# Performance work log

Measured on AMD Instinct MI355X. Metric: run time of the kernel, lower is better.

Reference implementation:

```python
import jax, jax.numpy as jnp
import numpy as np

N_T = 200
THR = 0.6
ALPHA = 0.8   # hard-coded in __init__
KAPPA = 0.8   # hard-coded in __init__
RHO = 0.97
BETA = 0.07
SCALE = 50.0  # get_pos scale
# norse defaults used by ConstantCurrentLIFEncoder / LILinearCell
DT = 1e-3
TAU_MEM_INV = 100.0
TAU_SYN_INV = 200.0
V_TH = 1.0


def encode_constant_current(I):
    """norse ConstantCurrentLIFEncoder: LIF driven by constant current I [n_b, f] -> spikes [n_t, n_b, f]."""
    def step(v, _):
        v = v + DT * TAU_MEM_INV * (I - v)          # dv = dt*tau_mem_inv*((v_leak - v) + I), v_leak=0
        z = (v > V_TH).astype(I.dtype)
        v = v * (1.0 - z)                            # reset to v_reset=0 on spike
        return v, z
    _, zs = jax.lax.scan(step, jnp.zeros_like(I), None, length=N_T)
    return zs


def setup_inputs() -> dict:
    key = jax.random.key(0)
    ks = jax.random.split(key, 5)
    n_b, n_feat = 128, 512
    n_in, n_rec, n_out = 2 * n_feat, 2048, 32
    x = jax.random.normal(ks[0], (n_b, n_feat), jnp.float32)
    # kaiming_normal_ std = sqrt(2/fan_in), then scaled by w_init_gain
    w_in = jax.random.normal(ks[1], (n_rec, n_in), jnp.float32) * (0.5 * np.sqrt(2.0 / n_in))
    w_rec = jax.random.normal(ks[2], (n_rec, n_rec), jnp.float32) * (0.1 * np.sqrt(2.0 / n_rec))
    w_out = jax.random.normal(ks[3], (n_out, n_rec), jnp.float32) * (0.5 * np.sqrt(2.0 / n_rec))
    w_li = jax.random.normal(ks[4], (1, n_rec), jnp.float32) * np.sqrt(2.0 / n_rec)
    return {"x": x, "w_in": w_in, "w_rec": w_rec, "w_out": w_out, "w_li": w_li}


def reference(x, w_in, w_rec, w_out, w_li):
    n_rec = w_rec.shape[0]
    n_out = w_out.shape[0]
    n_b = x.shape[0]
    # get_pos: pos/neg rectified constant-current LIF encoding, cat on feature dim -> [n_t, n_b, n_in]
    xs = jnp.concatenate([
        encode_constant_current(jax.nn.relu(SCALE * x)),
        encode_constant_current(jax.nn.relu(-SCALE * x)),
    ], axis=2)
    # zero self-recurrence: w_rec *= (1 - I)
    w_rec = w_rec * (1.0 - jnp.eye(n_rec, dtype=w_rec.dtype))

    def step(carry, x_t):
        v, a, z, vo, li_v, li_i = carry
        # ALIF membrane update + adaptive threshold spike
        v = ALPHA * v + z @ w_rec.T + x_t @ w_in.T - z * THR
        a = RHO * a + z
        z = (v > THR + BETA * a).astype(v.dtype)
        # (dropout p=0.5 treated as identity / eval mode)
        vo = KAPPA * vo + z @ w_out.T
        # norse LILinearCell critic readout (li_step)
        i_jump = li_i + z @ w_li.T
        li_v = li_v + DT * TAU_MEM_INV * (i_jump - li_v)
        li_i = i_jump - DT * TAU_SYN_INV * i_jump
        return (v, a, z, vo, li_v, li_i), (vo, li_v)

    zeros = lambda d: jnp.zeros((n_b, d), x.dtype)
    carry0 = (zeros(n_rec), zeros(n_rec), zeros(n_rec), zeros(n_out), zeros(1), zeros(1))
    _, (vo_seq, vc_seq) = jax.lax.scan(step, carry0, xs[: N_T - 1])  # loop runs n_t-1 steps
    # torch.max over time includes the all-zero t=0 row -> clamp max with 0
    m = jnp.maximum(jnp.max(vo_seq, axis=0), 0.0)          # [n_b, n_out]
    yo = jax.nn.softmax(m, axis=1)
    critic_value = jnp.maximum(jnp.max(vc_seq, axis=0), 0.0)  # [n_b, 1]
    return yo, critic_value
```

## Files before the change

kernel.cpp:

```cpp
#include <hip/hip_runtime.h>
#include <cstdint>
#include <cstddef>

typedef __attribute__((ext_vector_type(8))) short short8;
typedef __attribute__((ext_vector_type(4))) float f32x4;
typedef __attribute__((ext_vector_type(4))) unsigned int u32x4;

union U4S8 { u32x4 u; short8 s; unsigned w[4]; };

#define TSTEPS 199

#define WF_PLANE 786432u
#define WR_BASE  1572864u
#define WR_PLANE 12288u

#define WS_BAR  0u
#define WS_ZB   4096u
#define WS_FIN  135168u
#define WS_XSB  151552u
#define WS_WF   3411968u
#define WS_NEED 28971008u

#define AT_RLX __ATOMIC_RELAXED
#define SC_AGT __HIP_MEMORY_SCOPE_AGENT

extern "C" __global__ __launch_bounds__(1024) void k_encode(
    const float* __restrict__ x, unsigned char* __restrict__ xsb)
{
  const int b = blockIdx.x;
  const int tid = threadIdx.x;
  const float xv = (tid < 512) ? x[b * 512 + tid] : x[b * 512 + tid - 512];
  const float I = (tid < 512) ? fmaxf(__fmul_rn(50.0f, xv), 0.0f)
                              : fmaxf(__fmul_rn(-50.0f, xv), 0.0f);
  float v = 0.0f;
  unsigned long long* dst =
      (unsigned long long*)(xsb + (size_t)b * 128u + (size_t)(tid >> 6) * 8u);
  for (int t = 0; t < TSTEPS; ++t) {
    v = __fadd_rn(v, __fmul_rn(0.1f, __fsub_rn(I, v)));
    const bool z = v > 1.0f;
    if (z) v = 0.0f;
    const unsigned long long m = __ballot(z ? 1 : 0);
    if ((tid & 63) == 0) dst[(size_t)t * 2048u] = m;
  }
}

__device__ __forceinline__ unsigned bf16rne(float f) {
  const unsigned u = __float_as_uint(f);
  return ((u + 0x7FFFu + ((u >> 16) & 1u)) >> 16) & 0xFFFFu;
}

extern "C" __global__ __launch_bounds__(256) void k_prep(
    const float* __restrict__ w_rec, const float* __restrict__ w_in,
    const float* __restrict__ w_out, const float* __restrict__ w_li,
    u32x4* __restrict__ wf)
{
  const unsigned idx  = blockIdx.x * 256u + threadIdx.x;
  const unsigned lane = idx & 63u;
  if (idx < 786432u) {
    const unsigned kt = (idx >> 6) % 96u;
    const unsigned ns = idx / 6144u;
    const unsigned j  = ns * 16u + (lane & 15u);
    const unsigned k0 = kt * 32u + (lane >> 4) * 8u;
    unsigned hi[4], lo[4];
#pragma unroll
    for (int u2 = 0; u2 < 4; ++u2) {
      unsigned hb[2], lb[2];
#pragma unroll
      for (int c = 0; c < 2; ++c) {
        const unsigned k = k0 + 2u * (unsigned)u2 + (unsigned)c;
        float w;
        if (k < 2048u) w = (k == j) ? 0.0f : w_rec[(size_t)j * 2048u + k];
        else           w = w_in[(size_t)j * 1024u + (k - 2048u)];
        const unsigned h = bf16rne(w);
        const float hvf = __uint_as_float(h << 16);
        const unsigned l = bf16rne(__fsub_rn(w, hvf));
        hb[c] = h; lb[c] = l;
      }
      hi[u2] = hb[0] | (hb[1] << 16);
      lo[u2] = lb[0] | (lb[1] << 16);
    }
    u32x4 vh, vl;
    vh[0]=hi[0]; vh[1]=hi[1]; vh[2]=hi[2]; vh[3]=hi[3];
    vl[0]=lo[0]; vl[1]=lo[1]; vl[2]=lo[2]; vl[3]=lo[3];
    wf[idx] = vh;
    wf[idx + WF_PLANE] = vl;
  } else if (idx < 786432u + 12288u) {
    const unsigned r   = idx - 786432u;
    const unsigned kt  = (r >> 6) & 63u;
    const unsigned nsr = r >> 12;
    const unsigned o   = nsr * 16u + (lane & 15u);
    const unsigned k0  = kt * 32u + (lane >> 4) * 8u;
    unsigned hi[4], lo[4];
#pragma unroll
    for (int u2 = 0; u2 < 4; ++u2) {
      unsigned hb[2], lb[2];
#pragma unroll
      for (int c = 0; c < 2; ++c) {
        const unsigned k = k0 + 2u * (unsigned)u2 + (unsigned)c;
        float w = 0.0f;
        if (o < 32u)       w = w_out[(size_t)o * 2048u + k];
        else if (o == 32u) w = w_li[k];
        const unsigned h = bf16rne(w);
        const float hvf = __uint_as_float(h << 16);
        hb[c] = h;
        lb[c] = bf16rne(__fsub_rn(w, hvf));
      }
      hi[u2] = hb[0] | (hb[1] << 16);
      lo[u2] = lb[0] | (lb[1] << 16);
    }
    u32x4 vh, vl;
    vh[0]=hi[0]; vh[1]=hi[1]; vh[2]=hi[2]; vh[3]=hi[3];
    vl[0]=lo[0]; vl[1]=lo[1]; vl[2]=lo[2]; vl[3]=lo[3];
    wf[WR_BASE + r] = vh;
    wf[WR_BASE + WR_PLANE + r] = vl;
  }
}

__device__ __forceinline__ void bar_arrive(unsigned* dbar, unsigned ns)
{
  __syncthreads();
  if (threadIdx.x == 0) {
    const unsigned prev = __hip_atomic_fetch_add(dbar + (ns >> 4) * 16u, 1u, AT_RLX, SC_AGT);
    if ((prev & 15u) == 15u) {
      const unsigned p2 = __hip_atomic_fetch_add(dbar + 128u, 1u, AT_RLX, SC_AGT);
      if ((p2 & 7u) == 7u)
        __hip_atomic_store(dbar + 144u, (p2 >> 3) + 1u, AT_RLX, SC_AGT);
    }
  }
}

__device__ __forceinline__ void bar_wait(unsigned* dbar, unsigned tgt)
{
  if (threadIdx.x == 0) {
    while (__hip_atomic_load(dbar + 144u, AT_RLX, SC_AGT) < tgt) {
      __builtin_amdgcn_s_sleep(1);
    }
    asm volatile("" ::: "memory");
  }
  __syncthreads();
}

extern "C" __global__ __launch_bounds__(512) void k_main(
    const u32x4* __restrict__ wf,
    const unsigned char* __restrict__ xsb,
    unsigned* __restrict__ zb,
    unsigned* __restrict__ bar,
    unsigned* __restrict__ fin,
    float* __restrict__ out)
{
  __shared__ unsigned abytes[64][100];
  __shared__ float red[8][64][17];
  __shared__ unsigned char zn[64][4];
  __shared__ float pad_lds[6000];

  const unsigned tid  = threadIdx.x;
  const unsigned wg   = blockIdx.x;
  const unsigned mh   = wg >> 7;
  const unsigned ns   = wg & 127u;
  const unsigned wv   = tid >> 6;
  const unsigned lane = tid & 63u;
  const unsigned ln15 = lane & 15u;
  const unsigned g4   = lane >> 4;
  const unsigned selr = g4 * 0x01010101u;
  const unsigned blq  = tid & 63u;
  const unsigned q    = tid >> 6;
  const bool     upd  = tid < 256u;
  const bool     dual = ns < 3u;

  if (tid == 0) ((volatile float*)pad_lds)[0] = 0.f;

  unsigned* dbar = bar + mh * 256u;

  const u32x4* WH = wf + (size_t)ns * 6144u;
  const u32x4* WL = wf + WF_PLANE + (size_t)ns * 6144u;
  const u32x4* RH = wf + WR_BASE + (size_t)ns * 4096u;
  const u32x4* RL = wf + WR_BASE + WR_PLANE + (size_t)ns * 4096u;

  float v[4]  = {0,0,0,0}, a[4] = {0,0,0,0}, zf[4] = {0,0,0,0};
  float vo[4] = {0,0,0,0}, voMax[4] = {0,0,0,0};
  float liv = 0.f, lii = 0.f, liMax = 0.f;

  f32x4 accX0 = {0,0,0,0}, accX1 = {0,0,0,0}, accX2 = {0,0,0,0}, accX3 = {0,0,0,0};
  U4S8 bhZ[8], blZ[8];
  const int zk = (int)wv * 8;
  const int xk = 64 + (int)wv * 4;

  auto stage_z = [&](unsigned buf) {
    const unsigned base = (buf * 2u + mh) * 64u * 128u;
    for (unsigned i = tid; i < 4096u; i += 512u) {
      const unsigned row = i >> 6, np = i & 63u;
      const unsigned long long vz = __hip_atomic_load(
          (const unsigned long long*)(zb + base + row * 128u + np * 2u),
          AT_RLX, SC_AGT);
      abytes[row][np] = (unsigned)(vz & 0xFFFFu) | (unsigned)(((vz >> 32) & 0xFFFFu) << 16);
    }
  };

  auto stage_xs = [&](int t) {
    const unsigned char* xr = xsb + ((size_t)t * 128u + mh * 64u) * 128u;
    for (unsigned i = tid; i < 2048u; i += 512u) {
      const unsigned row = i >> 5, c = i & 31u;
      abytes[row][64u + c] = *(const unsigned*)(xr + (size_t)row * 128u + c * 4u);
    }
  };

  auto mk = [&](unsigned dw, U4S8& af) {
    const unsigned sp = __builtin_amdgcn_perm(dw, dw, selr);
    const unsigned W  = ((sp >> 1) & 0xFFFF0000u) | (sp & 0x0000FFFFu);
    af.w[0] = __umul24(W & 0x00010001u, 0x3F80u);
    af.w[1] = __umul24(W & 0x00040004u, 0x0FE0u);
    af.w[2] = __umul24(W & 0x00100010u, 0x03F8u);
    af.w[3] = __umul24(W & 0x00400040u, 0x00FEu);
  };

  auto dosub2 = [&](unsigned dw, const short8& bhj, const short8& blj, f32x4& ACC) {
    U4S8 af; mk(dw, af);
    ACC = __builtin_amdgcn_mfma_f32_16x16x32_bf16(af.s, bhj, ACC, 0, 0, 0);
    ACC = __builtin_amdgcn_mfma_f32_16x16x32_bf16(af.s, blj, ACC, 0, 0, 0);
  };

  auto ldw = [&](const u32x4* H, const u32x4* L, int kb, U4S8* bh, U4S8* bl) {
#pragma unroll
    for (int j = 0; j < 4; ++j) {
      bh[j].u = H[(size_t)(kb + j) * 64u + lane];
      bl[j].u = L[(size_t)(kb + j) * 64u + lane];
    }
  };

  auto grp4 = [&](int kb, const U4S8* bh, const U4S8* bl) {
    U4S8 a0, a1, a2, a3;
    a0.u = *(const u32x4*)&abytes[ 0 + ln15][kb];
    a1.u = *(const u32x4*)&abytes[16 + ln15][kb];
    a2.u = *(const u32x4*)&abytes[32 + ln15][kb];
    a3.u = *(const u32x4*)&abytes[48 + ln15][kb];
#pragma unroll
    for (int j = 0; j < 4; ++j) {
      dosub2(a0.w[j], bh[j].s, bl[j].s, accX0);
      dosub2(a1.w[j], bh[j].s, bl[j].s, accX1);
      dosub2(a2.w[j], bh[j].s, bl[j].s, accX2);
      dosub2(a3.w[j], bh[j].s, bl[j].s, accX3);
    }
  };

  auto compute_accX = [&]() {
    U4S8 bh2[4], bl2[4];
    accX0 = {0,0,0,0}; accX1 = {0,0,0,0}; accX2 = {0,0,0,0}; accX3 = {0,0,0,0};
    ldw(WH, WL, xk, bh2, bl2);
    grp4(xk, bh2, bl2);
  };

  auto prefetchZ = [&]() {
#pragma unroll
    for (int j = 0; j < 8; ++j) {
      bhZ[j].u = WH[(size_t)(zk + j) * 64u + lane];
      blZ[j].u = WL[(size_t)(zk + j) * 64u + lane];
    }
  };

  auto zpart = [&]() {
    grp4(zk,     &bhZ[0], &blZ[0]);
    grp4(zk + 4, &bhZ[4], &blZ[4]);
  };

  auto redstore = [&]() {
#pragma unroll
    for (int r = 0; r < 4; ++r) {
      red[wv][ 0 + g4 * 4 + r][ln15] = accX0[r];
      red[wv][16 + g4 * 4 + r][ln15] = accX1[r];
      red[wv][32 + g4 * 4 + r][ln15] = accX2[r];
      red[wv][48 + g4 * 4 + r][ln15] = accX3[r];
    }
  };

  auto readout_pass = [&]() {
    f32x4 r0 = {0,0,0,0}, r1 = {0,0,0,0}, r2 = {0,0,0,0}, r3 = {0,0,0,0};
    const int kb = (int)wv * 8;
#pragma unroll
    for (int kc = 0; kc < 8; kc += 4) {
      U4S8 ar0, ar1, ar2, ar3;
      ar0.u = *(const u32x4*)&abytes[ 0 + ln15][kb + kc];
      ar1.u = *(const u32x4*)&abytes[16 + ln15][kb + kc];
      ar2.u = *(const u32x4*)&abytes[32 + ln15][kb + kc];
      ar3.u = *(const u32x4*)&abytes[48 + ln15][kb + kc];
      U4S8 bh[4], bl[4];
#pragma unroll
      for (int j = 0; j < 4; ++j) {
        bh[j].u = RH[(size_t)(kb + kc + j) * 64u + lane];
        bl[j].u = RL[(size_t)(kb + kc + j) * 64u + lane];
      }
#pragma unroll
      for (int j = 0; j < 4; ++j) {
        dosub2(ar0.w[j], bh[j].s, bl[j].s, r0);
        dosub2(ar1.w[j], bh[j].s, bl[j].s, r1);
        dosub2(ar2.w[j], bh[j].s, bl[j].s, r2);
        dosub2(ar3.w[j], bh[j].s, bl[j].s, r3);
      }
    }
#pragma unroll
    for (int r = 0; r < 4; ++r) {
      red[wv][ 0 + g4 * 4 + r][ln15] = r0[r];
      red[wv][16 + g4 * 4 + r][ln15] = r1[r];
      red[wv][32 + g4 * 4 + r][ln15] = r2[r];
      red[wv][48 + g4 * 4 + r][ln15] = r3[r];
    }
    __syncthreads();
    if (upd) {
      if (ns < 2u) {
#pragma unroll
        for (int jj = 0; jj < 4; ++jj) {
          const unsigned n = q * 4u + (unsigned)jj;
          float s = ((red[0][blq][n] + red[1][blq][n]) + (red[2][blq][n] + red[3][blq][n]))
                  + ((red[4][blq][n] + red[5][blq][n]) + (red[6][blq][n] + red[7][blq][n]));
          vo[jj] = __fadd_rn(__fmul_rn(0.8f, vo[jj]), s);
          voMax[jj] = fmaxf(voMax[jj], vo[jj]);
        }
      } else if (q == 0u) {
        float s = ((red[0][blq][0] + red[1][blq][0]) + (red[2][blq][0] + red[3][blq][0]))
                + ((red[4][blq][0] + red[5][blq][0]) + (red[6][blq][0] + red[7][blq][0]));
        const float ij = __fadd_rn(lii, s);
        liv = __fadd_rn(liv, __fmul_rn(0.1f, __fsub_rn(ij, liv)));
        lii = __fsub_rn(ij, __fmul_rn(0.2f, ij));
        liMax = fmaxf(liMax, liv);
      }
    }
    __syncthreads();
  };

  stage_xs(0);
  __syncthreads();
  compute_accX();
  prefetchZ();

  for (int t = 0; t < TSTEPS; ++t) {
    if (t > 0) bar_wait(dbar, (unsigned)t);
    stage_z((unsigned)t & 1u);
    __syncthreads();

    zpart();
    redstore();
    __syncthreads();

    if (upd) {
      unsigned nib = 0u;
#pragma unroll
      for (int jj = 0; jj < 4; ++jj) {
        const unsigned n = q * 4u + (unsigned)jj;
        const float dv = ((red[0][blq][n] + red[1][blq][n]) + (red[2][blq][n] + red[3][blq][n]))
                       + ((red[4][blq][n] + red[5][blq][n]) + (red[6][blq][n] + red[7][blq][n]));
        const float vv = __fsub_rn(__fadd_rn(__fmul_rn(0.8f, v[jj]), dv),
                                   __fmul_rn(zf[jj], 0.6f));
        a[jj] = __fadd_rn(__fmul_rn(0.97f, a[jj]), zf[jj]);
        const float th = __fadd_rn(0.6f, __fmul_rn(0.07f, a[jj]));
        const bool znew = vv > th;
        zf[jj] = znew ? 1.0f : 0.0f;
        v[jj] = vv;
        nib |= (znew ? 1u : 0u) << jj;
      }
      zn[blq][q] = (unsigned char)nib;
    }
    __syncthreads();

    if (tid < 64u) {
      const unsigned m16 = (unsigned)zn[tid][0] | ((unsigned)zn[tid][1] << 4) |
                           ((unsigned)zn[tid][2] << 8) | ((unsigned)zn[tid][3] << 12);
      const unsigned nb = ((unsigned)t & 1u) ^ 1u;
      __hip_atomic_store(zb + ((nb * 2u + mh) * 64u + tid) * 128u + ns, m16,
                         AT_RLX, SC_AGT);
    }
    bar_arrive(dbar, ns);

    if (t < TSTEPS - 1) stage_xs(t + 1);
    if (dual && t > 0) readout_pass();
    __syncthreads();
    if (t < TSTEPS - 1) {
      compute_accX();
      prefetchZ();
    }
  }

  bar_wait(dbar, (unsigned)TSTEPS);
  if (dual) {
    stage_z((unsigned)TSTEPS & 1u);
    __syncthreads();
    readout_pass();
    if (ns < 2u && upd) {
#pragma unroll
      for (int jj = 0; jj < 4; ++jj) {
        __hip_atomic_store(fin + ((size_t)mh * 64u + blq) * 32u + ns * 16u + q * 4u + (unsigned)jj,
                           __float_as_uint(voMax[jj]), AT_RLX, SC_AGT);
      }
    }
    if (ns == 2u && tid < 64u) {
      out[4096u + mh * 64u + tid] = liMax;
    }
  }
  bar_arrive(dbar, ns);

  if (ns == 0u) {
    bar_wait(dbar, (unsigned)TSTEPS + 1u);
    if (tid < 64u) {
      const unsigned grow = mh * 64u + tid;
      float vals[32];
#pragma unroll
      for (int o = 0; o < 32; ++o)
        vals[o] = __uint_as_float(__hip_atomic_load(fin + (size_t)grow * 32u + o,
                                                    AT_RLX, SC_AGT));
      float mx = vals[0];
#pragma unroll
      for (int o = 1; o < 32; ++o) mx = fmaxf(mx, vals[o]);
      float ssum = 0.f;
#pragma unroll
      for (int o = 0; o < 32; ++o) ssum += expf(vals[o] - mx);
      const float inv = 1.0f / ssum;
#pragma unroll
      for (int o = 0; o < 32; ++o) out[(size_t)grow * 32u + o] = expf(vals[o] - mx) * inv;
    }
  }
}

extern "C" void kernel_launch(void* const* d_in, const int* in_sizes, int n_in,
                              void* d_out, int out_size, void* d_ws, size_t ws_size,
                              hipStream_t stream)
{
  (void)in_sizes; (void)n_in; (void)out_size;
  if (ws_size < (size_t)WS_NEED) return;

  const float* x     = (const float*)d_in[0];
  const float* w_in  = (const float*)d_in[1];
  const float* w_rec = (const float*)d_in[2];
  const float* w_out = (const float*)d_in[3];
  const float* w_li  = (const float*)d_in[4];
  unsigned char* ws  = (unsigned char*)d_ws;

  unsigned*      bar  = (unsigned*)(ws + WS_BAR);
  unsigned*      zb   = (unsigned*)(ws + WS_ZB);
  unsigned*      fin  = (unsigned*)(ws + WS_FIN);
  unsigned char* xsb  = ws + WS_XSB;
  u32x4*         wf   = (u32x4*)(ws + WS_WF);

  hipMemsetAsync(bar, 0, 4096, stream);
  hipMemsetAsync(zb, 0, 131072, stream);
  k_encode<<<dim3(128), dim3(1024), 0, stream>>>(x, xsb);
  k_prep<<<dim3(3120), dim3(256), 0, stream>>>(w_rec, w_in, w_out, w_li, wf);
  k_main<<<dim3(256), dim3(512), 0, stream>>>(wf, xsb, zb, bar, fin, (float*)d_out);
}
```

Baseline: 1.861 ms.

## Flatten grid barrier and fuse per-wave z staging into MFMA loop

Result: faster. 1.793 ms (-3.7%).

```diff
diff --git a/kernel.cpp b/kernel.cpp
--- a/kernel.cpp
+++ b/kernel.cpp
@@ -120,20 +120,22 @@
 {
   __syncthreads();
   if (threadIdx.x == 0) {
-    const unsigned prev = __hip_atomic_fetch_add(dbar + (ns >> 4) * 16u, 1u, AT_RLX, SC_AGT);
-    if ((prev & 15u) == 15u) {
-      const unsigned p2 = __hip_atomic_fetch_add(dbar + 128u, 1u, AT_RLX, SC_AGT);
-      if ((p2 & 7u) == 7u)
-        __hip_atomic_store(dbar + 144u, (p2 >> 3) + 1u, AT_RLX, SC_AGT);
-    }
-  }
-}
-
-__device__ __forceinline__ void bar_wait(unsigned* dbar, unsigned tgt)
+    __hip_atomic_fetch_add(dbar + (ns >> 4) * 16u, 1u, AT_RLX, SC_AGT);
+  }
+}
+
+__device__ __forceinline__ void bar_wait16(unsigned* dbar, unsigned tgt16)
 {
   if (threadIdx.x == 0) {
-    while (__hip_atomic_load(dbar + 144u, AT_RLX, SC_AGT) < tgt) {
-      __builtin_amdgcn_s_sleep(1);
+    for (;;) {
+      unsigned mn = 0xFFFFFFFFu;
+#pragma unroll
+      for (int g = 0; g < 8; ++g) {
+        const unsigned c = __hip_atomic_load(dbar + g * 16, AT_RLX, SC_AGT);
+        mn = (c < mn) ? c : mn;
+      }
+      if (mn >= tgt16) break;
+      __builtin_amdgcn_s_sleep(2);
     }
     asm volatile("" ::: "memory");
   }
@@ -185,23 +187,14 @@
   const int zk = (int)wv * 8;
   const int xk = 64 + (int)wv * 4;
 
-  auto stage_z = [&](unsigned buf) {
-    const unsigned base = (buf * 2u + mh) * 64u * 128u;
-    for (unsigned i = tid; i < 4096u; i += 512u) {
-      const unsigned row = i >> 6, np = i & 63u;
-      const unsigned long long vz = __hip_atomic_load(
-          (const unsigned long long*)(zb + base + row * 128u + np * 2u),
-          AT_RLX, SC_AGT);
-      abytes[row][np] = (unsigned)(vz & 0xFFFFu) | (unsigned)(((vz >> 32) & 0xFFFFu) << 16);
-    }
+  auto pk = [](unsigned long long t) -> unsigned {
+    return (unsigned)(t & 0xFFFFu) | (unsigned)(((t >> 32) & 0xFFFFu) << 16);
   };
 
   auto stage_xs = [&](int t) {
     const unsigned char* xr = xsb + ((size_t)t * 128u + mh * 64u) * 128u;
-    for (unsigned i = tid; i < 2048u; i += 512u) {
-      const unsigned row = i >> 5, c = i & 31u;
-      abytes[row][64u + c] = *(const unsigned*)(xr + (size_t)row * 128u + c * 4u);
-    }
+    const u32x4 val = *(const u32x4*)(xr + (size_t)lane * 128u + wv * 16u);
+    *(u32x4*)&abytes[lane][64u + wv * 4u] = val;
   };
 
   auto mk = [&](unsigned dw, U4S8& af) {
@@ -257,8 +250,22 @@
     }
   };
 
-  auto zpart = [&]() {
-    grp4(zk,     &bhZ[0], &blZ[0]);
+  auto stage_and_zpart = [&](unsigned buf) {
+    const unsigned long long* zp = (const unsigned long long*)zb +
+        ((size_t)((buf * 2u + mh) * 64u + lane) * 64u) + (unsigned)zk;
+    unsigned long long z0 = __hip_atomic_load(zp + 0, AT_RLX, SC_AGT);
+    unsigned long long z1 = __hip_atomic_load(zp + 1, AT_RLX, SC_AGT);
+    unsigned long long z2 = __hip_atomic_load(zp + 2, AT_RLX, SC_AGT);
+    unsigned long long z3 = __hip_atomic_load(zp + 3, AT_RLX, SC_AGT);
+    unsigned long long z4 = __hip_atomic_load(zp + 4, AT_RLX, SC_AGT);
+    unsigned long long z5 = __hip_atomic_load(zp + 5, AT_RLX, SC_AGT);
+    unsigned long long z6 = __hip_atomic_load(zp + 6, AT_RLX, SC_AGT);
+    unsigned long long z7 = __hip_atomic_load(zp + 7, AT_RLX, SC_AGT);
+    u32x4 wa; wa[0] = pk(z0); wa[1] = pk(z1); wa[2] = pk(z2); wa[3] = pk(z3);
+    *(u32x4*)&abytes[lane][(unsigned)zk] = wa;
+    grp4(zk, &bhZ[0], &blZ[0]);
+    u32x4 wb; wb[0] = pk(z4); wb[1] = pk(z5); wb[2] = pk(z6); wb[3] = pk(z7);
+    *(u32x4*)&abytes[lane][(unsigned)zk + 4u] = wb;
     grp4(zk + 4, &bhZ[4], &blZ[4]);
   };
 
@@ -290,10 +297,18 @@
       }
 #pragma unroll
       for (int j = 0; j < 4; ++j) {
-        dosub2(ar0.w[j], bh[j].s, bl[j].s, r0);
-        dosub2(ar1.w[j], bh[j].s, bl[j].s, r1);
-        dosub2(ar2.w[j], bh[j].s, bl[j].s, r2);
-        dosub2(ar3.w[j], bh[j].s, bl[j].s, r3);
+        U4S8 af0; mk(ar0.w[j], af0);
+        r0 = __builtin_amdgcn_mfma_f32_16x16x32_bf16(af0.s, bh[j].s, r0, 0, 0, 0);
+        r0 = __builtin_amdgcn_mfma_f32_16x16x32_bf16(af0.s, bl[j].s, r0, 0, 0, 0);
+        U4S8 af1; mk(ar1.w[j], af1);
+        r1 = __builtin_amdgcn_mfma_f32_16x16x32_bf16(af1.s, bh[j].s, r1, 0, 0, 0);
+        r1 = __builtin_amdgcn_mfma_f32_16x16x32_bf16(af1.s, bl[j].s, r1, 0, 0, 0);
+        U4S8 af2; mk(ar2.w[j], af2);
+        r2 = __builtin_amdgcn_mfma_f32_16x16x32_bf16(af2.s, bh[j].s, r2, 0, 0, 0);
+        r2 = __builtin_amdgcn_mfma_f32_16x16x32_bf16(af2.s, bl[j].s, r2, 0, 0, 0);
+        U4S8 af3; mk(ar3.w[j], af3);
+        r3 = __builtin_amdgcn_mfma_f32_16x16x32_bf16(af3.s, bh[j].s, r3, 0, 0, 0);
+        r3 = __builtin_amdgcn_mfma_f32_16x16x32_bf16(af3.s, bl[j].s, r3, 0, 0, 0);
       }
     }
 #pragma unroll
@@ -327,16 +342,13 @@
   };
 
   stage_xs(0);
-  __syncthreads();
   compute_accX();
   prefetchZ();
 
   for (int t = 0; t < TSTEPS; ++t) {
-    if (t > 0) bar_wait(dbar, (unsigned)t);
-    stage_z((unsigned)t & 1u);
-    __syncthreads();
-
-    zpart();
+    if (t > 0) bar_wait16(dbar, 16u * (unsigned)t);
+
+    stage_and_zpart((unsigned)t & 1u);
     redstore();
     __syncthreads();
 
@@ -371,17 +383,28 @@
 
     if (t < TSTEPS - 1) stage_xs(t + 1);
     if (dual && t > 0) readout_pass();
-    __syncthreads();
     if (t < TSTEPS - 1) {
       compute_accX();
       prefetchZ();
     }
   }
 
-  bar_wait(dbar, (unsigned)TSTEPS);
+  bar_wait16(dbar, 16u * (unsigned)TSTEPS);
   if (dual) {
-    stage_z((unsigned)TSTEPS & 1u);
-    __syncthreads();
+    const unsigned buf = (unsigned)TSTEPS & 1u;
+    const unsigned long long* zp = (const unsigned long long*)zb +
+        ((size_t)((buf * 2u + mh) * 64u + lane) * 64u) + (unsigned)zk;
+    u32x4 wa, wb;
+    wa[0] = pk(__hip_atomic_load(zp + 0, AT_RLX, SC_AGT));
+    wa[1] = pk(__hip_atomic_load(zp + 1, AT_RLX, SC_AGT));
+    wa[2] = pk(__hip_atomic_load(zp + 2, AT_RLX, SC_AGT));
+    wa[3] = pk(__hip_atomic_load(zp + 3, AT_RLX, SC_AGT));
+    wb[0] = pk(__hip_atomic_load(zp + 4, AT_RLX, SC_AGT));
+    wb[1] = pk(__hip_atomic_load(zp + 5, AT_RLX, SC_AGT));
+    wb[2] = pk(__hip_atomic_load(zp + 6, AT_RLX, SC_AGT));
+    wb[3] = pk(__hip_atomic_load(zp + 7, AT_RLX, SC_AGT));
+    *(u32x4*)&abytes[lane][(unsigned)zk] = wa;
+    *(u32x4*)&abytes[lane][(unsigned)zk + 4u] = wb;
     readout_pass();
     if (ns < 2u && upd) {
 #pragma unroll
@@ -397,7 +420,7 @@
   bar_arrive(dbar, ns);
 
   if (ns == 0u) {
-    bar_wait(dbar, (unsigned)TSTEPS + 1u);
+    bar_wait16(dbar, 16u * ((unsigned)TSTEPS + 1u));
     if (tid < 64u) {
       const unsigned grow = mh * 64u + tid;
       float vals[32];
```
